# Performance work log

Measured on AMD Instinct MI355X. Metric: run time of the kernel, lower is better.

## Reference

```python
import jax, jax.numpy as jnp
import numpy as np

BS, L, D, K, G, E = 512, 128, 512, 30, 8, 2048
H = E // 2  # MLP hidden = embed_dim // 2


def setup_inputs():
    key = jax.random.key(0)
    ks = jax.random.split(key, 8)
    features = jax.random.normal(ks[0], (BS, L, D), jnp.float32)
    atten = jax.random.uniform(ks[1], (BS, L, L), jnp.float32)
    rng = np.random.default_rng(0)
    lens = rng.integers(34, L - 1, size=BS)          # caption lengths (>= 34 so lengths-2 > K)
    toks = rng.integers(1, 1000, size=(BS, L))
    pos = np.arange(L)[None, :]
    text = np.where(pos < lens[:, None], toks, 0)    # zero padding
    text[np.arange(BS), lens - 1] = 49407            # eos = max token id -> argmax finds it
    text = jnp.asarray(text, jnp.int32)
    pid = jnp.asarray(np.repeat(np.arange(BS // G), G), jnp.int32)  # 64 groups of size G=8
    dlp_w = jax.random.normal(ks[2], (G, D), jnp.float32)           # weights['weight_8']
    dlp_b = jnp.zeros((G,), jnp.float32)                            # biases['bias_8']
    dlp_lw = jax.random.normal(ks[3], (K * G, E), jnp.float32) * 0.05  # linears['linear_8']
    dlp_lb = jnp.zeros((E,), jnp.float32)
    mlp_w1 = jax.random.normal(ks[4], (D, H), jnp.float32) * 0.04
    mlp_b1 = jnp.zeros((H,), jnp.float32)
    bn_g = jnp.ones((H,), jnp.float32)
    bn_b = jnp.zeros((H,), jnp.float32)
    mlp_w2 = jax.random.normal(ks[5], (H, E), jnp.float32) * 0.03
    mlp_b2 = jnp.zeros((E,), jnp.float32)
    return dict(features=features, atten=atten, text=text, pid=pid,
                dlp_w=dlp_w, dlp_b=dlp_b, dlp_lw=dlp_lw, dlp_lb=dlp_lb,
                mlp_w1=mlp_w1, mlp_b1=mlp_b1, bn_g=bn_g, bn_b=bn_b,
                mlp_w2=mlp_w2, mlp_b2=mlp_b2)


def _l2norm(x, eps=1e-8):
    return x / (jnp.sqrt(jnp.sum(x * x, axis=-1, keepdims=True)) + eps)


def _groups_from_pid(pid_np):
    # replicates the pid_dist==0 grouping + dedup-by-member-set, preserving first-seen order
    groups, order = {}, []
    for i, p in enumerate(pid_np.tolist()):
        if p not in groups:
            groups[p] = []
            order.append(p)
        groups[p].append(i)
    return [groups[p] for p in order]


def reference(features, atten, text, pid, dlp_w, dlp_b, dlp_lw, dlp_lb,
              mlp_w1, mlp_b1, bn_g, bn_b, mlp_w2, mlp_b2):
    bs = features.shape[0]
    b = jnp.arange(bs)
    mask = (text != 0).astype(features.dtype)                  # [bs, L]
    lengths = mask.sum(1) - 2.0                                # [bs]
    eos = jnp.argmax(text, axis=-1)                            # [bs]
    att = atten.at[b, :, eos].set(-1.0).at[:, :, 0].set(-1.0)
    row = att[b, eos, :] * mask                                # [bs, L]
    idx = jax.lax.top_k(row, K)[1]                             # [bs, K] topk token indices
    feats = jnp.take_along_axis(features, idx[:, :, None], axis=1)  # [bs, K, D]

    # pid-based dynamic grouping (host-side; pid is an index input, static)
    glists = _groups_from_pid(np.asarray(pid))
    assert {len(g) for g in glists} == {G}, 'expert params provided for group size G only'
    gi = np.asarray(glists)                                    # [ng, G]
    xg = feats[gi].reshape(gi.shape[0], G * K, D)              # concat group members: [ng, G*K, D]
    # F.linear(x, W[G,D], b).T  ->  [ng, G, G*K]
    h = jnp.einsum('ntd,gd->ngt', xg, dlp_w) + dlp_b[None, :, None]
    yg = h @ dlp_lw + dlp_lb                                   # linear_G: [ng, G, E]
    # scatter-combine each member's row back to its batch position
    new_base = jnp.zeros((bs, E), feats.dtype).at[gi.reshape(-1)].set(yg.reshape(-1, E))
    new_base = _l2norm(new_base)

    # MLP (Linear -> BatchNorm1d(train stats) -> ReLU -> Linear) on l2-normed gathered feats
    x = _l2norm(feats).reshape(bs * K, D) @ mlp_w1 + mlp_b1
    mu, var = x.mean(0), x.var(0)
    x = jax.nn.relu((x - mu) / jnp.sqrt(var + 1e-5) * bn_g + bn_b)
    x = (x @ mlp_w2 + mlp_b2).reshape(bs, K, E)

    # maxk_pool1d_var with pool k=1: per-channel max over first min(length, K) rows
    lens = jnp.minimum(lengths, K).astype(jnp.int32)
    valid = jnp.arange(K)[None, :] < lens[:, None]             # [bs, K]
    pooled = jnp.max(jnp.where(valid[:, :, None], x, -jnp.inf), axis=1)  # [bs, E]
    return (pooled + new_base).astype(jnp.float32)
```

## Files before the change

### kernel.cpp

```cpp
#include <hip/hip_runtime.h>
#include <hip/hip_bf16.h>

#define BS 512
#define LL 128
#define DD 512
#define KK 30
#define GG 8
#define EE 2048
#define HH 1024
#define NROWS (BS*KK)
#define NG (BS/GG)

typedef __attribute__((ext_vector_type(8))) short bf16x8;
typedef __attribute__((ext_vector_type(4))) float f32x4;
typedef __attribute__((address_space(1))) const unsigned int gu32;
typedef __attribute__((address_space(3))) unsigned int lu32;

__device__ __forceinline__ unsigned short f2bf(float f){
  unsigned int x = __float_as_uint(f);
  x = (x + 0x7FFFu + ((x >> 16) & 1u)) >> 16;
  return (unsigned short)x;
}
__device__ __forceinline__ float bf2f(unsigned short u){
  return __uint_as_float(((unsigned int)u) << 16);
}
__device__ __forceinline__ unsigned fkey(float f){
  unsigned b = __float_as_uint(f);
  return (b & 0x80000000u) ? ~b : (b | 0x80000000u);
}
__device__ __forceinline__ float fdec(unsigned k){
  unsigned b = (k & 0x80000000u) ? (k & 0x7FFFFFFFu) : ~k;
  return __uint_as_float(b);
}

#define FENCE asm volatile("" ::: "memory")
#define BARR  do{ FENCE; __builtin_amdgcn_s_barrier(); FENCE; }while(0)
#define LGK0  do{ asm volatile("s_waitcnt lgkmcnt(0)" ::: "memory"); \
                  __builtin_amdgcn_sched_barrier(0); }while(0)
#define VMW(n) asm volatile("s_waitcnt vmcnt(" #n ")" ::: "memory")

__global__ __launch_bounds__(256) void k_pg(const float* __restrict__ atten,
                                            const int* __restrict__ text,
                                            const float* __restrict__ features,
                                            const float* __restrict__ dlp_w,
                                            const float* __restrict__ dlp_b,
                                            const float* __restrict__ w1,
                                            unsigned short* __restrict__ w1t,
                                            unsigned short* __restrict__ nfeats,
                                            float* __restrict__ hval,
                                            int* __restrict__ lensk){
  __shared__ int sidx[KK];
  __shared__ float tile[32][33];

  if(blockIdx.x >= BS){
    const int blk = blockIdx.x - BS;
    const int n0 = (blk & 31)*32, k0 = (blk >> 5)*32;
    const int r = threadIdx.x >> 3, c4 = (threadIdx.x & 7)*4;
    const float4 v = *(const float4*)(w1 + (size_t)(k0 + r)*HH + n0 + c4);
    tile[r][c4+0] = v.x; tile[r][c4+1] = v.y; tile[r][c4+2] = v.z; tile[r][c4+3] = v.w;
    __syncthreads();
    ushort4 u;
    u.x = f2bf(tile[c4+0][r]); u.y = f2bf(tile[c4+1][r]);
    u.z = f2bf(tile[c4+2][r]); u.w = f2bf(tile[c4+3][r]);
    *(ushort4*)(w1t + (size_t)(n0 + r)*DD + k0 + c4) = u;
    return;
  }

  const int b = blockIdx.x;
  const int tid = threadIdx.x;
  const int wv = tid >> 6, lane = tid & 63;

  if(wv == 0){
    const int t0 = text[b*LL + lane];
    const int t1 = text[b*LL + 64 + lane];
    int v, vi;
    if(t1 > t0){ v = t1; vi = lane + 64; } else { v = t0; vi = lane; }
#pragma unroll
    for(int off = 32; off; off >>= 1){
      const int ov = __shfl_xor(v, off), oi = __shfl_xor(vi, off);
      if(ov > v || (ov == v && oi < vi)){ v = ov; vi = oi; }
    }
    const int eos = vi;
    const unsigned long long mb0 = __ballot(t0 != 0), mb1 = __ballot(t1 != 0);
    if(lane == 0) lensk[b] = min(__popcll(mb0) + __popcll(mb1) - 2, KK);

    const float a0 = atten[(size_t)b*LL*LL + (size_t)eos*LL + lane];
    const float a1 = atten[(size_t)b*LL*LL + (size_t)eos*LL + 64 + lane];
    float r0 = (t0 == 0) ? 0.f : ((lane == 0 || lane == eos) ? -1.f : a0);
    float r1 = (t1 == 0) ? 0.f : ((lane + 64 == eos) ? -1.f : a1);
    for(int k = 0; k < KK; k++){
      float mv; int mi;
      if(r1 > r0){ mv = r1; mi = lane + 64; } else { mv = r0; mi = lane; }
#pragma unroll
      for(int off = 32; off; off >>= 1){
        const float ov = __shfl_xor(mv, off); const int oi = __shfl_xor(mi, off);
        if(ov > mv || (ov == mv && oi < mi)){ mv = ov; mi = oi; }
      }
      if(lane == 0) sidx[k] = mi;
      if(mi == lane)      r0 = -3.f;
      if(mi == lane + 64) r1 = -3.f;
    }
  }
  __syncthreads();

  for(int it = 0; it < 8; it++){
    const int r = it*4 + wv;
    if(r >= KK) break;
    const int l = sidx[r];
    const float4* fp = (const float4*)features + ((size_t)b*LL + l)*(DD/4);
    const float4 v0 = fp[lane], v1 = fp[64 + lane];
    float ss = v0.x*v0.x + v0.y*v0.y + v0.z*v0.z + v0.w*v0.w
             + v1.x*v1.x + v1.y*v1.y + v1.z*v1.z + v1.w*v1.w;
#pragma unroll
    for(int off = 32; off; off >>= 1) ss += __shfl_xor(ss, off);
    float hout = 0.f;
#pragma unroll
    for(int g = 0; g < GG; g++){
      const float4 w0 = ((const float4*)dlp_w)[g*(DD/4) + lane];
      const float4 w1v = ((const float4*)dlp_w)[g*(DD/4) + 64 + lane];
      float hg = v0.x*w0.x + v0.y*w0.y + v0.z*w0.z + v0.w*w0.w
               + v1.x*w1v.x + v1.y*w1v.y + v1.z*w1v.z + v1.w*w1v.w;
#pragma unroll
      for(int off = 32; off; off >>= 1) hg += __shfl_xor(hg, off);
      if(lane == g) hout = hg;
    }
    if(lane < GG) hval[(size_t)(b*KK + r)*GG + lane] = hout + dlp_b[lane];
    const float rn = 1.0f / (sqrtf(ss) + 1e-8f);
    ushort4 u0, u1;
    u0.x = f2bf(v0.x*rn); u0.y = f2bf(v0.y*rn); u0.z = f2bf(v0.z*rn); u0.w = f2bf(v0.w*rn);
    u1.x = f2bf(v1.x*rn); u1.y = f2bf(v1.y*rn); u1.z = f2bf(v1.z*rn); u1.w = f2bf(v1.w*rn);
    ushort4* np = (ushort4*)nfeats + (size_t)(b*KK + r)*(DD/4);
    np[lane] = u0; np[64 + lane] = u1;
  }
}

__global__ __launch_bounds__(256) void k_dlp(const float* __restrict__ hval,
                                             const float* __restrict__ dlp_lw,
                                             const float* __restrict__ dlp_lb,
                                             unsigned short* __restrict__ nbbf){
  const int et = blockIdx.x;
  const int n  = blockIdx.y;
  const int tid = threadIdx.x;
  __shared__ float hs[GG][GG*KK];
  for(int i = tid; i < GG*GG*KK; i += 256){
    const int g = i / (GG*KK), tt = i % (GG*KK);
    const int m = tt / KK, kq = tt % KK;
    hs[g][tt] = hval[(size_t)(((n*GG + m)*KK) + kq)*GG + g];
  }
  __syncthreads();
  const int h = tid >> 7, c = tid & 127;
  const int e = et*128 + c;
  float acc[4] = {0.f, 0.f, 0.f, 0.f};
#pragma unroll 4
  for(int k = 0; k < GG*KK; k++){
    const float w = dlp_lw[(size_t)k*EE + e];
#pragma unroll
    for(int rr = 0; rr < 4; rr++) acc[rr] += hs[h*4 + rr][k] * w;
  }
  const float lb = dlp_lb[e];
#pragma unroll
  for(int rr = 0; rr < 4; rr++)
    nbbf[(size_t)(n*GG + h*4 + rr)*EE + e] = f2bf(acc[rr] + lb);
}

__global__ __launch_bounds__(256) void k_l2nb(unsigned short* __restrict__ nbbf){
  const int b = blockIdx.x, t = threadIdx.x;
  uint4* p = (uint4*)(nbbf + (size_t)b*EE);
  uint4 u = p[t];
  unsigned short* us = (unsigned short*)&u;
  float f[8]; float ss = 0.f;
#pragma unroll
  for(int j = 0; j < 8; j++){ f[j] = bf2f(us[j]); ss += f[j]*f[j]; }
#pragma unroll
  for(int off = 32; off > 0; off >>= 1) ss += __shfl_down(ss, off);
  __shared__ float red[4];
  __shared__ float s_rn;
  if((t & 63) == 0) red[t >> 6] = ss;
  __syncthreads();
  if(t == 0) s_rn = 1.0f / (sqrtf(red[0] + red[1] + red[2] + red[3]) + 1e-8f);
  __syncthreads();
  const float rn = s_rn;
#pragma unroll
  for(int j = 0; j < 8; j++) us[j] = f2bf(f[j]*rn);
  p[t] = u;
}

__global__ __launch_bounds__(256, 2) void k_g1(const unsigned short* __restrict__ A,
                                               const unsigned short* __restrict__ Bt,
                                               const float* __restrict__ bias,
                                               unsigned short* __restrict__ obf,
                                               float* __restrict__ psum,
                                               float* __restrict__ psq){
  const int KD = DD, ND = HH, NBX = HH/128;
  __shared__ short S[2][2][128*64];
  const int tid  = threadIdx.x;
  const int wave = tid >> 6, lane = tid & 63;
  const int wr = wave >> 1, wc = wave & 1;
  const int lrow = lane & 15, kg = lane >> 4;

  const int nwg = gridDim.x, cpx = nwg >> 3;
  const int bid = (blockIdx.x & 7)*cpx + (blockIdx.x >> 3);
  const int bx = bid % NBX, by = bid / NBX;
  const int m0 = by*128, n0 = bx*128;

  const unsigned short* Ab = A  + (size_t)m0*KD;
  const unsigned short* Bb = Bt + (size_t)n0*KD;

#define G1STG(tt, p) { \
  _Pragma("unroll") \
  for(int c = 0; c < 4; c++){ \
    const int i_ = tid + c*256; const int r_ = i_ >> 3; \
    const int g_ = (i_ & 7) ^ (r_ & 7); \
    __builtin_amdgcn_global_load_lds((gu32*)(Ab + (size_t)r_*KD + (tt)*64 + g_*8), \
                                     (lu32*)(&S[p][0][i_*8]), 16, 0, 0); \
  } \
  _Pragma("unroll") \
  for(int c = 0; c < 4; c++){ \
    const int i_ = tid + c*256; const int r_ = i_ >> 3; \
    const int g_ = (i_ & 7) ^ (r_ & 7); \
    __builtin_amdgcn_global_load_lds((gu32*)(Bb + (size_t)r_*KD + (tt)*64 + g_*8), \
                                     (lu32*)(&S[p][1][i_*8]), 16, 0, 0); \
  } \
}

  f32x4 acc[4][4] = {};
  const int NT = KD/64;
  G1STG(0, 0)
  G1STG(1, 1)

  const int arow = wr*64 + lrow;
  const int brow = wc*64 + lrow;
  const int gx0 = (kg       ^ (lrow & 7))*8;
  const int gx1 = ((4 + kg) ^ (lrow & 7))*8;

#pragma unroll 1
  for(int t = 0; t < NT; t++){
    const int p = t & 1;
    if(t < NT-1) VMW(8);
    else         VMW(0);
    BARR;
    const short* Abuf = &S[p][0][0];
    const short* Bbuf = &S[p][1][0];
    bf16x8 af[4], bg[4];
#pragma unroll
    for(int n = 0; n < 4; n++) bg[n] = *(const bf16x8*)(Bbuf + (brow + n*16)*64 + gx0);
#pragma unroll
    for(int m = 0; m < 4; m++) af[m] = *(const bf16x8*)(Abuf + (arow + m*16)*64 + gx0);
    __builtin_amdgcn_s_setprio(1);
#pragma unroll
    for(int m = 0; m < 4; m++)
#pragma unroll
      for(int n = 0; n < 4; n++)
        acc[m][n] = __builtin_amdgcn_mfma_f32_16x16x32_bf16(af[m], bg[n], acc[m][n], 0, 0, 0);
    __builtin_amdgcn_s_setprio(0);
#pragma unroll
    for(int n = 0; n < 4; n++) bg[n] = *(const bf16x8*)(Bbuf + (brow + n*16)*64 + gx1);
#pragma unroll
    for(int m = 0; m < 4; m++) af[m] = *(const bf16x8*)(Abuf + (arow + m*16)*64 + gx1);
    __builtin_amdgcn_s_setprio(1);
#pragma unroll
    for(int m = 0; m < 4; m++)
#pragma unroll
      for(int n = 0; n < 4; n++)
        acc[m][n] = __builtin_amdgcn_mfma_f32_16x16x32_bf16(af[m], bg[n], acc[m][n], 0, 0, 0);
    __builtin_amdgcn_s_setprio(0);
    BARR;
    if(t + 2 < NT){ G1STG(t+2, p) }
  }
#undef G1STG

  const int colb = n0 + wc*64 + lrow;
#pragma unroll
  for(int n = 0; n < 4; n++){
    const float bb = bias[colb + n*16];
    float sv = 0.f, qv = 0.f;
#pragma unroll
    for(int m = 0; m < 4; m++)
#pragma unroll
      for(int r = 0; r < 4; r++){
        const float v = acc[m][n][r] + bb; sv += v; qv += v*v;
      }
    sv += __shfl_xor(sv, 16); sv += __shfl_xor(sv, 32);
    qv += __shfl_xor(qv, 16); qv += __shfl_xor(qv, 32);
    if(lane < 16){
      psum[(size_t)(by*2 + wr)*ND + colb + n*16] = sv;
      psq [(size_t)(by*2 + wr)*ND + colb + n*16] = qv;
    }
#pragma unroll
    for(int m = 0; m < 4; m++){
      const int row = m0 + wr*64 + m*16 + kg*4;
#pragma unroll
      for(int r = 0; r < 4; r++)
        obf[(size_t)(row + r)*ND + colb + n*16] = f2bf(acc[m][n][r] + bb);
    }
  }
}

__global__ __launch_bounds__(256) void k_bnw(const float* __restrict__ psum,
                                             const float* __restrict__ psq,
                                             const float* __restrict__ bn_g,
                                             const float* __restrict__ bn_b,
                                             float* __restrict__ sc,
                                             float* __restrict__ sh,
                                             const float* __restrict__ w2,
                                             unsigned short* __restrict__ w2t){
  if(blockIdx.x < 4){
    const int c = blockIdx.x*256 + threadIdx.x;
    float s = 0.f, q = 0.f;
    for(int i = 0; i < 240; i++){ s += psum[(size_t)i*HH + c]; q += psq[(size_t)i*HH + c]; }
    const float mu  = s * (1.0f/NROWS);
    const float var = q * (1.0f/NROWS) - mu*mu;
    const float sv  = bn_g[c] / sqrtf(var + 1e-5f);
    sc[c] = sv;
    sh[c] = bn_b[c] - mu*sv;
    return;
  }
  __shared__ float tile[32][33];
  const int blk = blockIdx.x - 4;
  const int n0 = (blk & 63)*32, k0 = (blk >> 6)*32;
  const int r = threadIdx.x >> 3, c4 = (threadIdx.x & 7)*4;
  const float4 v = *(const float4*)(w2 + (size_t)(k0 + r)*EE + n0 + c4);
  tile[r][c4+0] = v.x; tile[r][c4+1] = v.y; tile[r][c4+2] = v.z; tile[r][c4+3] = v.w;
  __syncthreads();
  ushort4 u;
  u.x = f2bf(tile[c4+0][r]); u.y = f2bf(tile[c4+1][r]);
  u.z = f2bf(tile[c4+2][r]); u.w = f2bf(tile[c4+3][r]);
  *(ushort4*)(w2t + (size_t)(n0 + r)*HH + k0 + c4) = u;
}

__global__ __launch_bounds__(256) void k_bnrelu(unsigned short* __restrict__ x1,
                                                const float* __restrict__ sc,
                                                const float* __restrict__ sh,
                                                unsigned* __restrict__ pkey){
  const size_t i = (size_t)blockIdx.x*256 + threadIdx.x;
  const int c0 = (int)((i*8) & (HH-1));
  uint4 u = ((uint4*)x1)[i];
  unsigned short* us = (unsigned short*)&u;
  const float4 s0 = *(const float4*)(sc + c0), s1 = *(const float4*)(sc + c0 + 4);
  const float4 h0 = *(const float4*)(sh + c0), h1 = *(const float4*)(sh + c0 + 4);
  const float scv[8] = {s0.x,s0.y,s0.z,s0.w,s1.x,s1.y,s1.z,s1.w};
  const float shv[8] = {h0.x,h0.y,h0.z,h0.w,h1.x,h1.y,h1.z,h1.w};
#pragma unroll
  for(int j = 0; j < 8; j++)
    us[j] = f2bf(fmaxf(bf2f(us[j])*scv[j] + shv[j], 0.f));
  ((uint4*)x1)[i] = u;
  if(blockIdx.x < 1024)
    ((uint4*)pkey)[blockIdx.x*256 + threadIdx.x] =
        make_uint4(0x007FFFFFu, 0x007FFFFFu, 0x007FFFFFu, 0x007FFFFFu);
}

__global__ __launch_bounds__(512, 2) void k_g2(const unsigned short* __restrict__ A,
                                               const unsigned short* __restrict__ Bt,
                                               const int* __restrict__ lensk,
                                               unsigned* __restrict__ pkey){
  const int KD = HH, ND = EE, NBX = EE/256;
  __shared__ short S[2][2][256*64];
  const int tid  = threadIdx.x;
  const int wave = tid >> 6, lane = tid & 63;
  const int wr = wave >> 2, wc = wave & 3;
  const int lrow = lane & 15, kg = lane >> 4;

  const int nwg = gridDim.x, cpx = nwg >> 3;
  const int bid = (blockIdx.x & 7)*cpx + (blockIdx.x >> 3);
  const int bx = bid % NBX, by = bid / NBX;
  const int m0 = by*256, n0 = bx*256;

  const unsigned short* Ab = A  + (size_t)m0*KD;
  const unsigned short* Bb = Bt + (size_t)n0*KD;

#define STG_A(tt, p, c) { \
  const int i_ = tid + (c)*512; const int r_ = i_ >> 3; \
  const int g_ = (i_ & 7) ^ (r_ & 7); \
  __builtin_amdgcn_global_load_lds((gu32*)(Ab + (size_t)r_*KD + (tt)*64 + g_*8), \
                                   (lu32*)(&S[p][0][i_*8]), 16, 0, 0); }
#define STG_B(tt, p, c) { \
  const int i_ = tid + (c)*512; const int r_ = i_ >> 3; \
  const int g_ = (i_ & 7) ^ (r_ & 7); \
  __builtin_amdgcn_global_load_lds((gu32*)(Bb + (size_t)r_*KD + (tt)*64 + g_*8), \
                                   (lu32*)(&S[p][1][i_*8]), 16, 0, 0); }
#define DSR_B(gx)  _Pragma("unroll") for(int n = 0; n < 4; n++) \
    bg[n] = *(const bf16x8*)(Bbuf + (brow + n*16)*64 + (gx));
#define DSR_AL(gx) _Pragma("unroll") for(int m = 0; m < 4; m++) \
    af[m] = *(const bf16x8*)(Abuf + (arow + m*16)*64 + (gx));
#define DSR_AH(gx) _Pragma("unroll") for(int m = 0; m < 4; m++) \
    af[m] = *(const bf16x8*)(Abuf + (arow + 64 + m*16)*64 + (gx));
#define MFMA_L do{ __builtin_amdgcn_s_setprio(1); \
  _Pragma("unroll") for(int m = 0; m < 4; m++) \
  _Pragma("unroll") for(int n = 0; n < 4; n++) \
    acc[m][n] = __builtin_amdgcn_mfma_f32_16x16x32_bf16(af[m], bg[n], acc[m][n], 0, 0, 0); \
  __builtin_amdgcn_s_setprio(0); }while(0)
#define MFMA_H do{ __builtin_amdgcn_s_setprio(1); \
  _Pragma("unroll") for(int m = 0; m < 4; m++) \
  _Pragma("unroll") for(int n = 0; n < 4; n++) \
    acc[4+m][n] = __builtin_amdgcn_mfma_f32_16x16x32_bf16(af[m], bg[n], acc[4+m][n], 0, 0, 0); \
  __builtin_amdgcn_s_setprio(0); }while(0)

  f32x4 acc[8][4] = {};
  const int NT = KD/64;

  const int arow = wr*128 + lrow;
  const int brow = wc*64  + lrow;
  const int gx0 = (kg       ^ (lrow & 7))*8;
  const int gx1 = ((4 + kg) ^ (lrow & 7))*8;

  STG_A(0, 0, 0) STG_A(0, 0, 2)
  STG_B(0, 0, 0) STG_B(0, 0, 1) STG_B(0, 0, 2) STG_B(0, 0, 3)
  STG_A(0, 0, 1) STG_A(0, 0, 3)
  VMW(2); BARR;

#pragma unroll 1
  for(int t = 0; t < NT-1; t++){
    const int p = t & 1, q = p ^ 1;
    const short* Abuf = &S[p][0][0];
    const short* Bbuf = &S[p][1][0];
    bf16x8 bg[4], af[4];
    DSR_B(gx0); DSR_AL(gx0);
    STG_A(t+1, q, 0) STG_A(t+1, q, 2)
    VMW(2);
    BARR; LGK0;
    MFMA_L;
    BARR;
    DSR_AH(gx0);
    STG_B(t+1, q, 0) STG_B(t+1, q, 1)
    BARR; LGK0;
    MFMA_H;
    BARR;
    DSR_B(gx1); DSR_AL(gx1);
    STG_B(t+1, q, 2) STG_B(t+1, q, 3)
    BARR; LGK0;
    MFMA_L;
    BARR;
    DSR_AH(gx1);
    STG_A(t+1, q, 1) STG_A(t+1, q, 3)
    VMW(2);
    BARR; LGK0;
    MFMA_H;
    BARR;
  }
  {
    const int p = (NT-1) & 1;
    const short* Abuf = &S[p][0][0];
    const short* Bbuf = &S[p][1][0];
    bf16x8 bg[4], af[4];
    DSR_B(gx0); DSR_AL(gx0);
    VMW(0);
    BARR; LGK0;
    MFMA_L;
    BARR;
    DSR_AH(gx0);
    BARR; LGK0;
    MFMA_H;
    BARR;
    DSR_B(gx1); DSR_AL(gx1);
    BARR; LGK0;
    MFMA_L;
    BARR;
    DSR_AH(gx1);
    LGK0;
    MFMA_H;
  }
#undef STG_A
#undef STG_B
#undef DSR_B
#undef DSR_AL
#undef DSR_AH
#undef MFMA_L
#undef MFMA_H

  __syncthreads();
  unsigned* pool = (unsigned*)&S[0][0][0];
  const int b0 = m0 / KK;
  const int b1 = (m0 + 255) / KK;
  const int nseg = b1 - b0 + 1;
  for(int i = tid; i < nseg*256; i += 512) pool[i] = 0x007FFFFFu;
  __syncthreads();
  const int lcol = wc*64 + lrow;
  {
    int cur_b = -1;
    float mx[4];
#pragma unroll
    for(int m = 0; m < 8; m++){
#pragma unroll
      for(int r = 0; r < 4; r++){
        const int row = m0 + wr*128 + m*16 + kg*4 + r;
        const int bt = row / KK;
        const int rr = row - bt*KK;
        if(bt != cur_b){
          if(cur_b >= 0){
#pragma unroll
            for(int n = 0; n < 4; n++)
              atomicMax(&pool[(cur_b - b0)*256 + lcol + n*16], fkey(mx[n]));
          }
          cur_b = bt;
#pragma unroll
          for(int n = 0; n < 4; n++) mx[n] = -INFINITY;
        }
        if(rr < lensk[bt]){
#pragma unroll
          for(int n = 0; n < 4; n++) mx[n] = fmaxf(mx[n], acc[m][n][r]);
        }
      }
    }
#pragma unroll
    for(int n = 0; n < 4; n++)
      atomicMax(&pool[(cur_b - b0)*256 + lcol + n*16], fkey(mx[n]));
  }
  __syncthreads();
  for(int e = tid; e < nseg*256; e += 512){
    const int seg = e >> 8, col = e & 255;
    atomicMax(&pkey[(size_t)(b0 + seg)*ND + n0 + col], pool[e]);
  }
}

__global__ __launch_bounds__(256) void k_final(const unsigned* __restrict__ pkey,
                                               const float* __restrict__ b2,
                                               const unsigned short* __restrict__ nbbf,
                                               float* __restrict__ out){
  const size_t i = (size_t)blockIdx.x*256 + threadIdx.x;
  const int c0 = (int)((i*4) & (EE-1));
  const uint4 k = ((const uint4*)pkey)[i];
  const ushort4 nb4 = ((const ushort4*)nbbf)[i];
  const float4 b = *(const float4*)(b2 + c0);
  float4 o;
  o.x = fdec(k.x) + b.x + bf2f(nb4.x);
  o.y = fdec(k.y) + b.y + bf2f(nb4.y);
  o.z = fdec(k.z) + b.z + bf2f(nb4.z);
  o.w = fdec(k.w) + b.w + bf2f(nb4.w);
  ((float4*)out)[i] = o;
}

extern "C" void kernel_launch(void* const* d_in, const int* in_sizes, int n_in,
                              void* d_out, int out_size, void* d_ws, size_t ws_size,
                              hipStream_t stream){
  const float* features = (const float*)d_in[0];
  const float* atten    = (const float*)d_in[1];
  const int*   text     = (const int*)  d_in[2];
  const float* dlp_w    = (const float*)d_in[4];
  const float* dlp_b    = (const float*)d_in[5];
  const float* dlp_lw   = (const float*)d_in[6];
  const float* dlp_lb   = (const float*)d_in[7];
  const float* w1       = (const float*)d_in[8];
  const float* b1       = (const float*)d_in[9];
  const float* bn_g     = (const float*)d_in[10];
  const float* bn_b     = (const float*)d_in[11];
  const float* w2       = (const float*)d_in[12];
  const float* b2       = (const float*)d_in[13];
  float* out = (float*)d_out;

  char* ws = (char*)d_ws;
  float*          psum   = (float*)(ws + 0);
  float*          psq    = (float*)(ws + 983040);
  unsigned short* w1t    = (unsigned short*)(ws + 1966080);
  float*          hval   = (float*)(ws + 3014656);
  unsigned*       pkey   = (unsigned*)(ws + 0);
  int*            lensk  = (int*)(ws + 4194304);
  float*          sc     = (float*)(ws + 4196352);
  float*          sh     = (float*)(ws + 4200448);
  unsigned short* nfeats = (unsigned short*)(ws + 4204544);
  unsigned short* w2t    = (unsigned short*)(ws + 4204544);
  unsigned short* x1     = (unsigned short*)(ws + 19933184);
  unsigned short* nbbf   = (unsigned short*)(ws + 51390464);

  k_pg<<<BS + 512, 256, 0, stream>>>(atten, text, features, dlp_w, dlp_b,
                                     w1, w1t, nfeats, hval, lensk);
  k_dlp<<<dim3(16, NG), 256, 0, stream>>>(hval, dlp_lw, dlp_lb, nbbf);
  k_l2nb<<<BS, 256, 0, stream>>>(nbbf);
  k_g1<<<(HH/128)*(NROWS/128), 256, 0, stream>>>(nfeats, w1t, b1, x1, psum, psq);
  k_bnw<<<4 + 2048, 256, 0, stream>>>(psum, psq, bn_g, bn_b, sc, sh, w2, w2t);
  k_bnrelu<<<(NROWS*HH/8)/256, 256, 0, stream>>>(x1, sc, sh, pkey);
  k_g2<<<(EE/256)*(NROWS/256), 512, 0, stream>>>(x1, w2t, lensk, pkey);
  k_final<<<(BS*EE/4)/256, 256, 0, stream>>>(pkey, b2, nbbf, out);
}
```

Baseline: 183.0 us.

## Shrink second GEMM tile to 128x128 with simpler double-buffered pipeline

Replaces the 256x256-tile, 512-thread second MLP GEMM with a 128x128-tile, 256-thread version. The finely interleaved staging schedule is replaced by a simpler loop that issues the global-to-LDS loads two k-steps ahead. That means one barrier pair per k-step instead of many barriers and lgkmcnt waits. The smaller tiles give four times as many workgroups and less LDS per block, which should help occupancy and load balance. In exchange each tile reuses data less, so global and L2 traffic rises, and the pooled atomicMax epilogue handles more, smaller segments.

```diff
diff --git a/kernel.cpp b/kernel.cpp
--- a/kernel.cpp
+++ b/kernel.cpp
@@ -35,8 +35,6 @@
 
 #define FENCE asm volatile("" ::: "memory")
 #define BARR  do{ FENCE; __builtin_amdgcn_s_barrier(); FENCE; }while(0)
-#define LGK0  do{ asm volatile("s_waitcnt lgkmcnt(0)" ::: "memory"); \
-                  __builtin_amdgcn_sched_barrier(0); }while(0)
 #define VMW(n) asm volatile("s_waitcnt vmcnt(" #n ")" ::: "memory")
 
 __global__ __launch_bounds__(256) void k_pg(const float* __restrict__ atten,
@@ -349,147 +347,111 @@
         make_uint4(0x007FFFFFu, 0x007FFFFFu, 0x007FFFFFu, 0x007FFFFFu);
 }
 
-__global__ __launch_bounds__(512, 2) void k_g2(const unsigned short* __restrict__ A,
+__global__ __launch_bounds__(256, 2) void k_g2(const unsigned short* __restrict__ A,
                                                const unsigned short* __restrict__ Bt,
                                                const int* __restrict__ lensk,
                                                unsigned* __restrict__ pkey){
-  const int KD = HH, ND = EE, NBX = EE/256;
-  __shared__ short S[2][2][256*64];
+  const int KD = HH, ND = EE, NBX = EE/128;
+  __shared__ short S[2][2][128*64];
   const int tid  = threadIdx.x;
   const int wave = tid >> 6, lane = tid & 63;
-  const int wr = wave >> 2, wc = wave & 3;
+  const int wr = wave >> 1, wc = wave & 1;
   const int lrow = lane & 15, kg = lane >> 4;
 
   const int nwg = gridDim.x, cpx = nwg >> 3;
   const int bid = (blockIdx.x & 7)*cpx + (blockIdx.x >> 3);
   const int bx = bid % NBX, by = bid / NBX;
-  const int m0 = by*256, n0 = bx*256;
+  const int m0 = by*128, n0 = bx*128;
 
   const unsigned short* Ab = A  + (size_t)m0*KD;
   const unsigned short* Bb = Bt + (size_t)n0*KD;
 
-#define STG_A(tt, p, c) { \
-  const int i_ = tid + (c)*512; const int r_ = i_ >> 3; \
-  const int g_ = (i_ & 7) ^ (r_ & 7); \
-  __builtin_amdgcn_global_load_lds((gu32*)(Ab + (size_t)r_*KD + (tt)*64 + g_*8), \
-                                   (lu32*)(&S[p][0][i_*8]), 16, 0, 0); }
-#define STG_B(tt, p, c) { \
-  const int i_ = tid + (c)*512; const int r_ = i_ >> 3; \
-  const int g_ = (i_ & 7) ^ (r_ & 7); \
-  __builtin_amdgcn_global_load_lds((gu32*)(Bb + (size_t)r_*KD + (tt)*64 + g_*8), \
-                                   (lu32*)(&S[p][1][i_*8]), 16, 0, 0); }
-#define DSR_B(gx)  _Pragma("unroll") for(int n = 0; n < 4; n++) \
-    bg[n] = *(const bf16x8*)(Bbuf + (brow + n*16)*64 + (gx));
-#define DSR_AL(gx) _Pragma("unroll") for(int m = 0; m < 4; m++) \
-    af[m] = *(const bf16x8*)(Abuf + (arow + m*16)*64 + (gx));
-#define DSR_AH(gx) _Pragma("unroll") for(int m = 0; m < 4; m++) \
-    af[m] = *(const bf16x8*)(Abuf + (arow + 64 + m*16)*64 + (gx));
-#define MFMA_L do{ __builtin_amdgcn_s_setprio(1); \
-  _Pragma("unroll") for(int m = 0; m < 4; m++) \
-  _Pragma("unroll") for(int n = 0; n < 4; n++) \
-    acc[m][n] = __builtin_amdgcn_mfma_f32_16x16x32_bf16(af[m], bg[n], acc[m][n], 0, 0, 0); \
-  __builtin_amdgcn_s_setprio(0); }while(0)
-#define MFMA_H do{ __builtin_amdgcn_s_setprio(1); \
-  _Pragma("unroll") for(int m = 0; m < 4; m++) \
-  _Pragma("unroll") for(int n = 0; n < 4; n++) \
-    acc[4+m][n] = __builtin_amdgcn_mfma_f32_16x16x32_bf16(af[m], bg[n], acc[4+m][n], 0, 0, 0); \
-  __builtin_amdgcn_s_setprio(0); }while(0)
-
-  f32x4 acc[8][4] = {};
+#define G2STG(tt, p) { \
+  _Pragma("unroll") \
+  for(int c = 0; c < 4; c++){ \
+    const int i_ = tid + c*256; const int r_ = i_ >> 3; \
+    const int g_ = (i_ & 7) ^ (r_ & 7); \
+    __builtin_amdgcn_global_load_lds((gu32*)(Ab + (size_t)r_*KD + (tt)*64 + g_*8), \
+                                     (lu32*)(&S[p][0][i_*8]), 16, 0, 0); \
+  } \
+  _Pragma("unroll") \
+  for(int c = 0; c < 4; c++){ \
+    const int i_ = tid + c*256; const int r_ = i_ >> 3; \
+    const int g_ = (i_ & 7) ^ (r_ & 7); \
+    __builtin_amdgcn_global_load_lds((gu32*)(Bb + (size_t)r_*KD + (tt)*64 + g_*8), \
+                                     (lu32*)(&S[p][1][i_*8]), 16, 0, 0); \
+  } \
+}
+
+  f32x4 acc[4][4] = {};
   const int NT = KD/64;
-
-  const int arow = wr*128 + lrow;
-  const int brow = wc*64  + lrow;
+  G2STG(0, 0)
+  G2STG(1, 1)
+
+  const int arow = wr*64 + lrow;
+  const int brow = wc*64 + lrow;
   const int gx0 = (kg       ^ (lrow & 7))*8;
   const int gx1 = ((4 + kg) ^ (lrow & 7))*8;
 
-  STG_A(0, 0, 0) STG_A(0, 0, 2)
-  STG_B(0, 0, 0) STG_B(0, 0, 1) STG_B(0, 0, 2) STG_B(0, 0, 3)
-  STG_A(0, 0, 1) STG_A(0, 0, 3)
-  VMW(2); BARR;
-
 #pragma unroll 1
-  for(int t = 0; t < NT-1; t++){
-    const int p = t & 1, q = p ^ 1;
+  for(int t = 0; t < NT; t++){
+    const int p = t & 1;
+    if(t < NT-1) VMW(8);
+    else         VMW(0);
+    BARR;
     const short* Abuf = &S[p][0][0];
     const short* Bbuf = &S[p][1][0];
-    bf16x8 bg[4], af[4];
-    DSR_B(gx0); DSR_AL(gx0);
-    STG_A(t+1, q, 0) STG_A(t+1, q, 2)
-    VMW(2);
-    BARR; LGK0;
-    MFMA_L;
+    bf16x8 af[4], bg[4];
+#pragma unroll
+    for(int n = 0; n < 4; n++) bg[n] = *(const bf16x8*)(Bbuf + (brow + n*16)*64 + gx0);
+#pragma unroll
+    for(int m = 0; m < 4; m++) af[m] = *(const bf16x8*)(Abuf + (arow + m*16)*64 + gx0);
+    __builtin_amdgcn_s_setprio(1);
+#pragma unroll
+    for(int m = 0; m < 4; m++)
+#pragma unroll
+      for(int n = 0; n < 4; n++)
+        acc[m][n] = __builtin_amdgcn_mfma_f32_16x16x32_bf16(af[m], bg[n], acc[m][n], 0, 0, 0);
+    __builtin_amdgcn_s_setprio(0);
+#pragma unroll
+    for(int n = 0; n < 4; n++) bg[n] = *(const bf16x8*)(Bbuf + (brow + n*16)*64 + gx1);
+#pragma unroll
+    for(int m = 0; m < 4; m++) af[m] = *(const bf16x8*)(Abuf + (arow + m*16)*64 + gx1);
+    __builtin_amdgcn_s_setprio(1);
+#pragma unroll
+    for(int m = 0; m < 4; m++)
+#pragma unroll
+      for(int n = 0; n < 4; n++)
+        acc[m][n] = __builtin_amdgcn_mfma_f32_16x16x32_bf16(af[m], bg[n], acc[m][n], 0, 0, 0);
+    __builtin_amdgcn_s_setprio(0);
     BARR;
-    DSR_AH(gx0);
-    STG_B(t+1, q, 0) STG_B(t+1, q, 1)
-    BARR; LGK0;
-    MFMA_H;
-    BARR;
-    DSR_B(gx1); DSR_AL(gx1);
-    STG_B(t+1, q, 2) STG_B(t+1, q, 3)
-    BARR; LGK0;
-    MFMA_L;
-    BARR;
-    DSR_AH(gx1);
-    STG_A(t+1, q, 1) STG_A(t+1, q, 3)
-    VMW(2);
-    BARR; LGK0;
-    MFMA_H;
-    BARR;
-  }
-  {
-    const int p = (NT-1) & 1;
-    const short* Abuf = &S[p][0][0];
-    const short* Bbuf = &S[p][1][0];
-    bf16x8 bg[4], af[4];
-    DSR_B(gx0); DSR_AL(gx0);
-    VMW(0);
-    BARR; LGK0;
-    MFMA_L;
-    BARR;
-    DSR_AH(gx0);
-    BARR; LGK0;
-    MFMA_H;
-    BARR;
-    DSR_B(gx1); DSR_AL(gx1);
-    BARR; LGK0;
-    MFMA_L;
-    BARR;
-    DSR_AH(gx1);
-    LGK0;
-    MFMA_H;
-  }
-#undef STG_A
-#undef STG_B
-#undef DSR_B
-#undef DSR_AL
-#undef DSR_AH
-#undef MFMA_L
-#undef MFMA_H
+    if(t + 2 < NT){ G2STG(t+2, p) }
+  }
+#undef G2STG
 
   __syncthreads();
   unsigned* pool = (unsigned*)&S[0][0][0];
   const int b0 = m0 / KK;
-  const int b1 = (m0 + 255) / KK;
+  const int b1 = (m0 + 127) / KK;
   const int nseg = b1 - b0 + 1;
-  for(int i = tid; i < nseg*256; i += 512) pool[i] = 0x007FFFFFu;
+  for(int i = tid; i < nseg*128; i += 256) pool[i] = 0x007FFFFFu;
   __syncthreads();
   const int lcol = wc*64 + lrow;
   {
     int cur_b = -1;
     float mx[4];
 #pragma unroll
-    for(int m = 0; m < 8; m++){
+    for(int m = 0; m < 4; m++){
 #pragma unroll
       for(int r = 0; r < 4; r++){
-        const int row = m0 + wr*128 + m*16 + kg*4 + r;
+        const int row = m0 + wr*64 + m*16 + kg*4 + r;
         const int bt = row / KK;
         const int rr = row - bt*KK;
         if(bt != cur_b){
           if(cur_b >= 0){
 #pragma unroll
             for(int n = 0; n < 4; n++)
-              atomicMax(&pool[(cur_b - b0)*256 + lcol + n*16], fkey(mx[n]));
+              atomicMax(&pool[(cur_b - b0)*128 + lcol + n*16], fkey(mx[n]));
           }
           cur_b = bt;
 #pragma unroll
@@ -503,11 +465,11 @@
     }
 #pragma unroll
     for(int n = 0; n < 4; n++)
-      atomicMax(&pool[(cur_b - b0)*256 + lcol + n*16], fkey(mx[n]));
-  }
-  __syncthreads();
-  for(int e = tid; e < nseg*256; e += 512){
-    const int seg = e >> 8, col = e & 255;
+      atomicMax(&pool[(cur_b - b0)*128 + lcol + n*16], fkey(mx[n]));
+  }
+  __syncthreads();
+  for(int e = tid; e < nseg*128; e += 256){
+    const int seg = e >> 7, col = e & 127;
     atomicMax(&pkey[(size_t)(b0 + seg)*ND + n0 + col], pool[e]);
   }
 }
@@ -568,6 +530,6 @@
   k_g1<<<(HH/128)*(NROWS/128), 256, 0, stream>>>(nfeats, w1t, b1, x1, psum, psq);
   k_bnw<<<4 + 2048, 256, 0, stream>>>(psum, psq, bn_g, bn_b, sc, sh, w2, w2t);
   k_bnrelu<<<(NROWS*HH/8)/256, 256, 0, stream>>>(x1, sc, sh, pkey);
-  k_g2<<<(EE/256)*(NROWS/256), 512, 0, stream>>>(x1, w2t, lensk, pkey);
+  k_g2<<<(EE/128)*(NROWS/128), 256, 0, stream>>>(x1, w2t, lensk, pkey);
   k_final<<<(BS*EE/4)/256, 256, 0, stream>>>(pkey, b2, nbbf, out);
 }
```

New measurement: 192.3 us. 5.1% more time.
